# Kernel tuning notes

Hardware: AMD Instinct MI355X
Metric: run time of the kernel (lower is better)

The kernel has to match this reference:

```python
import jax, jax.numpy as jnp
import numpy as np

B, S, HIDDEN = 2, 2048, 1024
NUM_HEADS, HEAD_DIM = 16, 64
STRIDE = 128
NEG = -10000.0


def _strided_mask(seq_len):
    # Sparse Transformer strided pattern: causal, local window of STRIDE,
    # plus every STRIDE-th previous position.
    i = jnp.arange(seq_len)[:, None]
    j = jnp.arange(seq_len)[None, :]
    diff = i - j
    allowed = (diff >= 0) & ((diff < STRIDE) | (diff % STRIDE == 0))
    return jnp.where(allowed, 0.0, NEG).astype(jnp.float32)  # [S, S]


def setup_inputs() -> dict:
    key = jax.random.key(0)
    k0, k1, k2, k3, k4 = jax.random.split(key, 5)
    hidden_states = jax.random.normal(k0, (B, S, HIDDEN), dtype=jnp.float32)
    attention_mask = jnp.zeros((B, 1, 1, S), dtype=jnp.float32)
    W_q = jax.random.normal(k1, (HIDDEN, HIDDEN), dtype=jnp.float32) * 0.02
    b_q = jnp.zeros((HIDDEN,), dtype=jnp.float32)
    W_v = jax.random.normal(k2, (HIDDEN, HIDDEN), dtype=jnp.float32) * 0.02
    b_v = jnp.zeros((HIDDEN,), dtype=jnp.float32)
    return {"hidden_states": hidden_states, "attention_mask": attention_mask,
            "W_q": W_q, "b_q": b_q, "W_v": W_v, "b_v": b_v}


def _heads(x):
    b, s, _ = x.shape
    return x.reshape(b, s, NUM_HEADS, HEAD_DIM).transpose(0, 2, 1, 3)  # [B,H,S,d]


def reference(hidden_states, attention_mask, W_q, b_q, W_v, b_v):
    q = _heads(hidden_states @ W_q + b_q)  # [B,H,S,d]
    v = _heads(hidden_states @ W_v + b_v)  # [B,H,S,d]
    hash_mask = _strided_mask(q.shape[-2])  # [S,S], broadcast over B,H
    # NB: source computes matmul(query, query^T) -- Q used for both sides.
    scores = jnp.einsum('bhid,bhjd->bhij', q, q) + hash_mask
    scores = scores / jnp.sqrt(jnp.asarray(HEAD_DIM, scores.dtype))
    scores = scores + attention_mask
    probs = jax.nn.softmax(scores, axis=-1)  # dropout p=0 (eval)
    ctx = jnp.einsum('bhij,bhjd->bhid', probs, v)  # [B,H,S,d]
    b = ctx.shape[0]
    return ctx.transpose(0, 2, 1, 3).reshape(b, -1, NUM_HEADS * HEAD_DIM)
```

## Files before the change

kernel.cpp:

```cpp
#include <hip/hip_runtime.h>

typedef __attribute__((ext_vector_type(8))) short short8;
typedef __attribute__((ext_vector_type(4))) float float4v;

__device__ inline float bf2f(ushort u) {
    unsigned v = ((unsigned)u) << 16;
    return __builtin_bit_cast(float, v);
}
__device__ inline ushort f2bf(float f) {
    unsigned u = __builtin_bit_cast(unsigned, f);
    u += 0x7FFFu + ((u >> 16) & 1u);
    return (ushort)(u >> 16);
}

__device__ inline void gload_lds16(const ushort* g, ushort* l) {
    __builtin_amdgcn_global_load_lds(
        (const __attribute__((address_space(1))) unsigned int*)g,
        (__attribute__((address_space(3))) unsigned int*)l,
        16, 0, 0);
}

__global__ __launch_bounds__(256) void prep(
    const float* __restrict__ hs, ushort* __restrict__ hsb,
    const float* __restrict__ Wq, const float* __restrict__ Wv,
    ushort* __restrict__ Wt) {
    __shared__ ushort tile[64][68];
    if (blockIdx.x < 1024) {
        const size_t base = ((size_t)blockIdx.x * 256 + threadIdx.x) * 16;
        union { ushort u[16]; uint4 v[2]; } o;
#pragma unroll
        for (int q = 0; q < 4; ++q) {
            float4v f = *(const float4v*)(hs + base + q * 4);
#pragma unroll
            for (int j = 0; j < 4; ++j) o.u[q * 4 + j] = f2bf(f[j]);
        }
        *(uint4*)(hsb + base)     = o.v[0];
        *(uint4*)(hsb + base + 8) = o.v[1];
        return;
    }
    const int idx = blockIdx.x - 1024;
    const int z = idx >> 8, yy = (idx >> 4) & 15, xx = idx & 15;
    const float* W = z ? Wv : Wq;
    ushort* Wto    = Wt + (z ? (size_t)1024 * 1024 : 0);
    const int k0 = yy * 64, n0 = xx * 64;
    const int tid = threadIdx.x;
    const int rr = tid >> 4;
    const int cc = (tid & 15) * 4;
    union U4 { ushort u[4]; uint2 v; };
#pragma unroll
    for (int i = 0; i < 4; ++i) {
        int row = rr + i * 16;
        float4v f = *(const float4v*)(W + (size_t)(k0 + row) * 1024 + n0 + cc);
        U4 x;
#pragma unroll
        for (int j = 0; j < 4; ++j) x.u[j] = f2bf(f[j]);
        *(uint2*)&tile[row][cc] = x.v;
    }
    __syncthreads();
#pragma unroll
    for (int i = 0; i < 4; ++i) {
        int row = rr + i * 16;
        U4 o;
#pragma unroll
        for (int j = 0; j < 4; ++j) o.u[j] = tile[cc + j][row];
        *(uint2*)(Wto + (size_t)(n0 + row) * 1024 + k0 + cc) = o.v;
    }
}

__global__ __launch_bounds__(512, 2) void qv_gemm(
    const ushort* __restrict__ hsb, const ushort* __restrict__ Wt,
    const float* __restrict__ bq, const float* __restrict__ bv,
    ushort* __restrict__ q_ws, ushort* __restrict__ v_ws) {
    __shared__ ushort smem[73728];
    const int wg = blockIdx.x;
    const int n0 = (wg & 7) * 256;
    const int m0 = (wg >> 3) * 128;
    const int tid  = threadIdx.x;
    const int wid  = tid >> 6, lane = tid & 63;
    const int quad = lane >> 4, l16 = lane & 15;
    const int wm = (wid >> 2) * 64;
    const int wn = (wid & 3) * 64;
    const int srow8 = tid >> 3;
    const int scb   = (tid & 7) * 16;

    auto stage = [&](int ktt, int bi, int r) {
        if (r < 2) {
            int row = r * 64 + srow8;
            int sb  = scb ^ ((row & 7) << 4);
            gload_lds16(hsb + (size_t)(m0 + row) * 1024 + ktt * 64 + (sb >> 1),
                        (ushort*)((char*)smem + bi * 49152 + r * 8192 + wid * 1024));
        } else {
            int row = (r - 2) * 64 + srow8;
            int sb  = scb ^ ((row & 7) << 4);
            gload_lds16(Wt + (size_t)(n0 + row) * 1024 + ktt * 64 + (sb >> 1),
                        (ushort*)((char*)smem + bi * 49152 + 16384 + (r - 2) * 8192 + wid * 1024));
        }
    };

    float4v acc[4][4] = {};

#pragma unroll
    for (int r = 0; r < 6; ++r) stage(0, 0, r);
#pragma unroll
    for (int r = 0; r < 6; ++r) stage(1, 1, r);

    int bi = 0;
    for (int ktt = 0; ktt < 16; ++ktt) {
        const char* Ab = (const char*)smem + bi * 49152;
        const char* Bb = Ab + 16384;

        if (ktt < 15) asm volatile("s_waitcnt vmcnt(6)" ::: "memory");
        else          asm volatile("s_waitcnt vmcnt(0)" ::: "memory");
        __builtin_amdgcn_s_barrier();
        __builtin_amdgcn_sched_barrier(0);

        short8 af[4][2], bfr[4][2];
#pragma unroll
        for (int mt = 0; mt < 4; ++mt) {
            int ar = wm + mt * 16 + l16;
            int sw = (ar & 7) << 4;
            af[mt][0] = *(const short8*)(Ab + ar * 128 + ((quad * 16) ^ sw));
        }
#pragma unroll
        for (int nt = 0; nt < 4; ++nt) {
            int br = wn + nt * 16 + l16;
            int sw = (br & 7) << 4;
            bfr[nt][0] = *(const short8*)(Bb + br * 128 + ((quad * 16) ^ sw));
        }
        __builtin_amdgcn_sched_barrier(0);
        const int kn = ktt + 2;
        const int b2 = (bi + 2 >= 3) ? bi - 1 : bi + 2;
        if (kn < 16) {
            stage(kn, b2, 0); stage(kn, b2, 1); stage(kn, b2, 2);
            stage(kn, b2, 3); stage(kn, b2, 4); stage(kn, b2, 5);
        }
#pragma unroll
        for (int mt = 0; mt < 4; ++mt) {
            int ar = wm + mt * 16 + l16;
            int sw = (ar & 7) << 4;
            af[mt][1] = *(const short8*)(Ab + ar * 128 + (((4 + quad) * 16) ^ sw));
        }
#pragma unroll
        for (int nt = 0; nt < 4; ++nt) {
            int br = wn + nt * 16 + l16;
            int sw = (br & 7) << 4;
            bfr[nt][1] = *(const short8*)(Bb + br * 128 + (((4 + quad) * 16) ^ sw));
        }
        __builtin_amdgcn_sched_barrier(0);
        asm volatile("s_waitcnt lgkmcnt(8)" ::: "memory");
        __builtin_amdgcn_sched_barrier(0);
        __builtin_amdgcn_s_setprio(1);
#pragma unroll
        for (int mt = 0; mt < 4; ++mt)
#pragma unroll
            for (int nt = 0; nt < 4; ++nt)
                acc[mt][nt] = __builtin_amdgcn_mfma_f32_16x16x32_bf16(
                    af[mt][0], bfr[nt][0], acc[mt][nt], 0, 0, 0);
        __builtin_amdgcn_s_setprio(0);
        asm volatile("s_waitcnt lgkmcnt(0)" ::: "memory");
        __builtin_amdgcn_sched_barrier(0);
        __builtin_amdgcn_s_setprio(1);
#pragma unroll
        for (int mt = 0; mt < 4; ++mt)
#pragma unroll
            for (int nt = 0; nt < 4; ++nt)
                acc[mt][nt] = __builtin_amdgcn_mfma_f32_16x16x32_bf16(
                    af[mt][1], bfr[nt][1], acc[mt][nt], 0, 0, 0);
        __builtin_amdgcn_s_setprio(0);

        bi = (bi + 1 >= 3) ? 0 : bi + 1;
    }

#pragma unroll
    for (int mt = 0; mt < 4; ++mt) {
#pragma unroll
        for (int nt = 0; nt < 4; ++nt) {
            int coln = n0 + wn + nt * 16 + l16;
            bool isq = coln < 1024;
            int c2 = isq ? coln : coln - 1024;
            float bsv = isq ? bq[c2] : bv[c2];
            ushort* outp = isq ? q_ws : v_ws;
            int hh = c2 >> 6, dd = c2 & 63;
#pragma unroll
            for (int reg = 0; reg < 4; ++reg) {
                int r = m0 + wm + mt * 16 + quad * 4 + reg;
                int bb = r >> 11, s = r & 2047;
                outp[(((size_t)bb * 16 + hh) * 2048 + s) * 64 + dd] =
                    f2bf(acc[mt][nt][reg] + bsv);
            }
        }
    }
}

#define SISSUE(As, Bs, Ms, idx) { const ushort* kr_ = q_ws + srbase + ((size_t)(idx) << 13); \
    As = *(const uint4*)kr_; Bs = *(const uint4*)(kr_ + 8); Ms = amask[amrow + ((idx) << 7)]; }
#define SCONS(As, Bs, Ms, kk) { union { uint4 v; ushort u[8]; } t0_, t1_; t0_.v = As; t1_.v = Bs; \
    float p_ = 0.f; \
    _Pragma("unroll") for (int jj = 0; jj < 8; ++jj) p_ += qv[jj] * bf2f(t0_.u[jj]); \
    _Pragma("unroll") for (int jj = 0; jj < 8; ++jj) p_ += qv[8 + jj] * bf2f(t1_.u[jj]); \
    p_ += __shfl_xor(p_, 1); p_ += __shfl_xor(p_, 2); \
    if ((tid & 3) == 0) Sstr[sr][kk] = p_ * 0.125f + Ms; }
#define VISSUE(As, Bs, idx) { const ushort* vr_ = v_ws + srbase + ((size_t)(idx) << 13); \
    As = *(const uint4*)vr_; Bs = *(const uint4*)(vr_ + 8); }
#define VCONS(As, Bs, kk) { float p_ = Sstr[sr][kk]; union { uint4 v; ushort u[8]; } t0_, t1_; \
    t0_.v = As; t1_.v = Bs; \
    _Pragma("unroll") for (int jj = 0; jj < 8; ++jj) acc16[jj] += p_ * bf2f(t0_.u[jj]); \
    _Pragma("unroll") for (int jj = 0; jj < 8; ++jj) acc16[8 + jj] += p_ * bf2f(t1_.u[jj]); }

__global__ __launch_bounds__(512, 4) void attn(
    const ushort* __restrict__ q_ws, const ushort* __restrict__ v_ws,
    const float* __restrict__ amask, float* __restrict__ out) {
    const int wg = blockIdx.x;
    const int half = wg >> 8, r5 = wg & 255;
    const int t_raw = r5 & 15;
    const int t = half ? (15 - t_raw) : t_raw;
    const int h = r5 >> 4;
    const int b = half;

    __shared__ ushort KwPl[16384];
    __shared__ ushort VtS[16384];
    __shared__ float  Sstr[128][17];
    __shared__ float  amw[256];

    const int tid = threadIdx.x;
    const int wid = tid >> 6, lane = tid & 63;
    const int quad = lane >> 4, l16 = lane & 15;
    const int r0 = wid * 16;
    const size_t qbase = ((size_t)b * 16 + h) * 2048 * 64;
    const int base_row = (t - 1) * 128;
    const int nk = (t >= 2) ? (t - 1) : 0;

    const int sr = tid >> 2;
    const int dq = (tid & 3) * 16;
    const size_t srbase = qbase + (size_t)sr * 64 + dq;
    const size_t amrow  = (size_t)b * 2048 + sr;

#pragma unroll
    for (int i = 0; i < 4; ++i) {
        int u = tid + i * 512;
        int row = u >> 3, c = u & 7;
        int jg = base_row + row; if (jg < 0) jg = 0;
        int sc = c ^ (row & 7);
        gload_lds16(q_ws + qbase + (size_t)jg * 64 + sc * 8, &KwPl[u * 8]);
    }
    __builtin_amdgcn_sched_barrier(0);

    {
        const int vj = tid & 255, dh0 = (tid >> 8) * 32;
        int vjg = base_row + vj; if (vjg < 0) vjg = 0;
        const ushort* vsrc = v_ws + qbase + (size_t)vjg * 64 + dh0;
        int cj = vj >> 3, j7 = vj & 7;
#pragma unroll
        for (int d0 = 0; d0 < 32; d0 += 8) {
            union { uint4 v; ushort u[8]; } tmp;
            tmp.v = *(const uint4*)(vsrc + d0);
#pragma unroll
            for (int jj = 0; jj < 8; ++jj) {
                int dd = dh0 + d0 + jj;
                VtS[dd * 256 + ((cj ^ (dd & 7)) * 8) + j7] = tmp.u[jj];
            }
        }
        int amj = base_row + (tid & 255); if (amj < 0) amj = 0;
        amw[tid & 255] = amask[(size_t)b * 2048 + amj];
    }

    uint4 kA0{}, kB0{}, kA1{}, kB1{}, kA2{}, kB2{};
    float am0 = 0.f, am1 = 0.f, am2 = 0.f;
    if (nk > 0) {
        SISSUE(kA0, kB0, am0, 0);
        SISSUE(kA1, kB1, am1, (1 < nk ? 1 : 0));
        SISSUE(kA2, kB2, am2, (2 < nk ? 2 : 0));
    }

    asm volatile("s_waitcnt vmcnt(0) lgkmcnt(0)" ::: "memory");
    __builtin_amdgcn_s_barrier();
    __builtin_amdgcn_sched_barrier(0);

    if (nk > 0) {
        float qv[16];
#pragma unroll
        for (int cc = 0; cc < 2; ++cc) {
            int c = (dq >> 3) + cc;
            union { uint4 v; ushort u[8]; } tm;
            tm.v = *(const uint4*)&KwPl[(128 + sr) * 64 + ((c ^ (sr & 7)) * 8)];
#pragma unroll
            for (int jj = 0; jj < 8; ++jj) qv[cc * 8 + jj] = bf2f(tm.u[jj]);
        }
        for (int k = 0; k < nk; k += 3) {
            SCONS(kA0, kB0, am0, k);
            if (k + 3 < nk) SISSUE(kA0, kB0, am0, k + 3);
            if (k + 1 < nk) {
                SCONS(kA1, kB1, am1, k + 1);
                if (k + 4 < nk) SISSUE(kA1, kB1, am1, k + 4);
            }
            if (k + 2 < nk) {
                SCONS(kA2, kB2, am2, k + 2);
                if (k + 5 < nk) SISSUE(kA2, kB2, am2, k + 5);
            }
        }
    }

    float4v sacc[16] = {};
    __builtin_amdgcn_s_setprio(1);
#pragma unroll
    for (int ks = 0; ks < 2; ++ks) {
        int c = ks * 4 + quad;
        int sw = (c ^ (l16 & 7)) * 8;
        short8 af = *(const short8*)&KwPl[(128 + r0 + l16) * 64 + sw];
#pragma unroll
        for (int nt = 0; nt < 16; ++nt) {
            short8 bfr = *(const short8*)&KwPl[(nt * 16 + l16) * 64 + sw];
            sacc[nt] = __builtin_amdgcn_mfma_f32_16x16x32_bf16(af, bfr, sacc[nt], 0, 0, 0);
        }
    }
    __builtin_amdgcn_s_setprio(0);
    __syncthreads();

    unsigned pb[4][4];
#pragma unroll
    for (int reg = 0; reg < 4; ++reg) {
        int rr = r0 + quad * 4 + reg;
        float sstr_v = (l16 < nk) ? Sstr[rr][l16] : -INFINITY;
        float m = sstr_v;
#pragma unroll
        for (int nt = 0; nt < 16; ++nt) {
            int c = nt * 16 + l16;
            bool allowed = (c >= rr) && (c <= rr + 128) && (t > 0 || c >= 128);
            float x = allowed ? sacc[nt][reg] * 0.125f + amw[c] : -INFINITY;
            sacc[nt][reg] = x;
            m = fmaxf(m, x);
        }
#pragma unroll
        for (int off = 1; off < 16; off <<= 1) m = fmaxf(m, __shfl_xor(m, off));

        float es = (l16 < nk) ? __expf(sstr_v - m) : 0.f;
        float sum = es;
#pragma unroll
        for (int nt = 0; nt < 16; ++nt) {
            float x = sacc[nt][reg];
            float e = (x == -INFINITY) ? 0.f : __expf(x - m);
            sacc[nt][reg] = e; sum += e;
        }
#pragma unroll
        for (int off = 1; off < 16; off <<= 1) sum += __shfl_xor(sum, off);
        float rden = 1.f / sum;
#pragma unroll
        for (int nt = 0; nt < 8; ++nt) {
            int c = nt * 2 + (l16 >> 3);
            KwPl[rr * 128 + ((c ^ (rr & 15)) * 8) + (l16 & 7)] = f2bf(sacc[nt][reg] * rden);
        }
#pragma unroll
        for (int i2 = 0; i2 < 4; ++i2) {
            unsigned lo = f2bf(sacc[8 + 2 * i2][reg] * rden);
            unsigned hi = f2bf(sacc[9 + 2 * i2][reg] * rden);
            pb[reg][i2] = lo | (hi << 16);
        }
        if (l16 < nk) Sstr[rr][l16] = es * rden;
    }
    __syncthreads();

    uint4 vA0{}, vB0{}, vA1{}, vB1{}, vA2{}, vB2{};
    if (nk > 0) {
        VISSUE(vA0, vB0, 0);
        VISSUE(vA1, vB1, (1 < nk ? 1 : 0));
        VISSUE(vA2, vB2, (2 < nk ? 2 : 0));
    }

    float4v cacc[4] = {};
    __builtin_amdgcn_s_setprio(1);
#pragma unroll
    for (int ks = 0; ks < 4; ++ks) {
        int cp = ks * 4 + quad;
        short8 af = *(const short8*)&KwPl[(r0 + l16) * 128 + ((cp ^ l16) * 8)];
#pragma unroll
        for (int nt = 0; nt < 4; ++nt) {
            int sw = (cp ^ (l16 & 7)) * 8;
            short8 bfr = *(const short8*)&VtS[(nt * 16 + l16) * 256 + sw];
            cacc[nt] = __builtin_amdgcn_mfma_f32_16x16x32_bf16(af, bfr, cacc[nt], 0, 0, 0);
        }
    }
    __builtin_amdgcn_s_setprio(0);
    __syncthreads();

#pragma unroll
    for (int reg = 0; reg < 4; ++reg) {
        int rr = r0 + quad * 4 + reg;
#pragma unroll
        for (int i2 = 0; i2 < 4; ++i2) {
            int nt0 = 8 + 2 * i2;
#pragma unroll
            for (int e2 = 0; e2 < 2; ++e2) {
                int nt = nt0 + e2;
                int c = (nt - 8) * 2 + (l16 >> 3);
                ushort val = (ushort)((pb[reg][i2] >> (16 * e2)) & 0xFFFF);
                KwPl[rr * 128 + ((c ^ (rr & 15)) * 8) + (l16 & 7)] = val;
            }
        }
    }
    __syncthreads();

    __builtin_amdgcn_s_setprio(1);
#pragma unroll
    for (int ks = 0; ks < 4; ++ks) {
        int cp = ks * 4 + quad;
        short8 af = *(const short8*)&KwPl[(r0 + l16) * 128 + ((cp ^ l16) * 8)];
#pragma unroll
        for (int nt = 0; nt < 4; ++nt) {
            int cv = 16 + cp;
            int sw = (cv ^ (l16 & 7)) * 8;
            short8 bfr = *(const short8*)&VtS[(nt * 16 + l16) * 256 + sw];
            cacc[nt] = __builtin_amdgcn_mfma_f32_16x16x32_bf16(af, bfr, cacc[nt], 0, 0, 0);
        }
    }
    __builtin_amdgcn_s_setprio(0);

    float acc16[16] = {};
    if (nk > 0) {
        for (int k = 0; k < nk; k += 3) {
            VCONS(vA0, vB0, k);
            if (k + 3 < nk) VISSUE(vA0, vB0, k + 3);
            if (k + 1 < nk) {
                VCONS(vA1, vB1, k + 1);
                if (k + 4 < nk) VISSUE(vA1, vB1, k + 4);
            }
            if (k + 2 < nk) {
                VCONS(vA2, vB2, k + 2);
                if (k + 5 < nk) VISSUE(vA2, vB2, k + 5);
            }
        }
    }
    __syncthreads();

    float* ctxp = (float*)&VtS[0];
#pragma unroll
    for (int d4 = 0; d4 < 4; ++d4) {
        int c = (dq >> 2) + d4;
        *(float4v*)&ctxp[sr * 64 + ((c ^ (sr & 15)) * 4)] =
            *(const float4v*)&acc16[d4 * 4];
    }
    __syncthreads();

    const size_t obase = ((size_t)b * 2048 + (size_t)t * 128) * 1024 + (size_t)h * 64;
#pragma unroll
    for (int nt = 0; nt < 4; ++nt)
#pragma unroll
        for (int reg = 0; reg < 4; ++reg) {
            int rr = r0 + quad * 4 + reg;
            int d = nt * 16 + l16;
            float cstr = ctxp[rr * 64 + (((d >> 2) ^ (rr & 15)) * 4) + (d & 3)];
            out[obase + (size_t)rr * 1024 + d] = cacc[nt][reg] + cstr;
        }
}

extern "C" void kernel_launch(void* const* d_in, const int* in_sizes, int n_in,
                              void* d_out, int out_size, void* d_ws, size_t ws_size,
                              hipStream_t stream) {
    int ihs = -1, iam = -1, iw1 = -1, iw2 = -1, ib1 = -1, ib2 = -1;
    for (int i = 0; i < n_in; ++i) {
        int s = in_sizes[i];
        if      (s == 4194304) { if (ihs < 0) ihs = i; }
        else if (s == 4096)    { if (iam < 0) iam = i; }
        else if (s == 1048576) { if (iw1 < 0) iw1 = i; else if (iw2 < 0) iw2 = i; }
        else if (s == 1024)    { if (ib1 < 0) ib1 = i; else if (ib2 < 0) ib2 = i; }
    }
    if (ihs < 0) ihs = 0; if (iam < 0) iam = 1;
    if (iw1 < 0) iw1 = 2; if (ib1 < 0) ib1 = 3;
    if (iw2 < 0) iw2 = 4; if (ib2 < 0) ib2 = 5;

    const float* hs    = (const float*)d_in[ihs];
    const float* amask = (const float*)d_in[iam];
    const float* Wq    = (const float*)d_in[iw1];
    const float* bq    = (const float*)d_in[ib1];
    const float* Wv    = (const float*)d_in[iw2];
    const float* bv    = (const float*)d_in[ib2];
    float* out = (float*)d_out;

    char* ws = (char*)d_ws;
    ushort* Wt   = (ushort*)(ws);
    ushort* hsb  = (ushort*)(ws + (1u << 22));
    ushort* q_ws = (ushort*)(ws + (1u << 22) + (1u << 23));
    ushort* v_ws = (ushort*)(ws + (1u << 22) + (2u << 23));

    prep<<<1536, 256, 0, stream>>>(hs, hsb, Wq, Wv, Wt);
    qv_gemm<<<256, 512, 0, stream>>>(hsb, Wt, bq, bv, q_ws, v_ws);
    attn<<<512, 512, 0, stream>>>(q_ws, v_ws, amask, out);
}
```

Baseline: 132.6 us.

## Split QV projection GEMM k-step into interleaved quadrant phases with staggered prefetch

Restructures the inner k-loop of the fused Q/V projection GEMM into four quadrant phases. Each phase loads a subset of A/B fragments from LDS, issues a third of the global-to-LDS prefetch for tile k+2, and runs its MFMAs behind block barriers, in a ping-pong style schedule. The aim is to spread LDS reads and global loads across the MFMA work so they overlap more evenly and stall less. In exchange it adds three extra s_barriers and full lgkmcnt(0) waits per iteration, which could serialize the waves.

```diff
diff --git a/kernel.cpp b/kernel.cpp
--- a/kernel.cpp
+++ b/kernel.cpp
@@ -108,6 +108,9 @@
     for (int ktt = 0; ktt < 16; ++ktt) {
         const char* Ab = (const char*)smem + bi * 49152;
         const char* Bb = Ab + 16384;
+        const int kn = ktt + 2;
+        const int b2 = (bi + 2 >= 3) ? bi - 1 : bi + 2;
+        const bool pf = (kn < 16);
 
         if (ktt < 15) asm volatile("s_waitcnt vmcnt(6)" ::: "memory");
         else          asm volatile("s_waitcnt vmcnt(0)" ::: "memory");
@@ -115,57 +118,94 @@
         __builtin_amdgcn_sched_barrier(0);
 
         short8 af[4][2], bfr[4][2];
-#pragma unroll
-        for (int mt = 0; mt < 4; ++mt) {
+
+#pragma unroll
+        for (int mt = 0; mt < 2; ++mt) {
             int ar = wm + mt * 16 + l16;
             int sw = (ar & 7) << 4;
             af[mt][0] = *(const short8*)(Ab + ar * 128 + ((quad * 16) ^ sw));
-        }
-#pragma unroll
-        for (int nt = 0; nt < 4; ++nt) {
+            af[mt][1] = *(const short8*)(Ab + ar * 128 + (((4 + quad) * 16) ^ sw));
+        }
+#pragma unroll
+        for (int nt = 0; nt < 2; ++nt) {
             int br = wn + nt * 16 + l16;
             int sw = (br & 7) << 4;
             bfr[nt][0] = *(const short8*)(Bb + br * 128 + ((quad * 16) ^ sw));
-        }
-        __builtin_amdgcn_sched_barrier(0);
-        const int kn = ktt + 2;
-        const int b2 = (bi + 2 >= 3) ? bi - 1 : bi + 2;
-        if (kn < 16) {
-            stage(kn, b2, 0); stage(kn, b2, 1); stage(kn, b2, 2);
-            stage(kn, b2, 3); stage(kn, b2, 4); stage(kn, b2, 5);
-        }
-#pragma unroll
-        for (int mt = 0; mt < 4; ++mt) {
+            bfr[nt][1] = *(const short8*)(Bb + br * 128 + (((4 + quad) * 16) ^ sw));
+        }
+        if (pf) { stage(kn, b2, 0); stage(kn, b2, 1); }
+        __builtin_amdgcn_sched_barrier(0);
+        __builtin_amdgcn_s_barrier();
+        asm volatile("s_waitcnt lgkmcnt(0)" ::: "memory");
+        __builtin_amdgcn_sched_barrier(0);
+        __builtin_amdgcn_s_setprio(1);
+#pragma unroll
+        for (int ks = 0; ks < 2; ++ks)
+#pragma unroll
+            for (int mt = 0; mt < 2; ++mt)
+#pragma unroll
+                for (int nt = 0; nt < 2; ++nt)
+                    acc[mt][nt] = __builtin_amdgcn_mfma_f32_16x16x32_bf16(
+                        af[mt][ks], bfr[nt][ks], acc[mt][nt], 0, 0, 0);
+        __builtin_amdgcn_s_setprio(0);
+        __builtin_amdgcn_sched_barrier(0);
+        __builtin_amdgcn_s_barrier();
+
+#pragma unroll
+        for (int nt = 2; nt < 4; ++nt) {
+            int br = wn + nt * 16 + l16;
+            int sw = (br & 7) << 4;
+            bfr[nt][0] = *(const short8*)(Bb + br * 128 + ((quad * 16) ^ sw));
+            bfr[nt][1] = *(const short8*)(Bb + br * 128 + (((4 + quad) * 16) ^ sw));
+        }
+        if (pf) { stage(kn, b2, 2); stage(kn, b2, 3); }
+        __builtin_amdgcn_sched_barrier(0);
+        __builtin_amdgcn_s_barrier();
+        asm volatile("s_waitcnt lgkmcnt(0)" ::: "memory");
+        __builtin_amdgcn_sched_barrier(0);
+        __builtin_amdgcn_s_setprio(1);
+#pragma unroll
+        for (int ks = 0; ks < 2; ++ks)
+#pragma unroll
+            for (int mt = 0; mt < 2; ++mt)
+#pragma unroll
+                for (int nt = 2; nt < 4; ++nt)
+                    acc[mt][nt] = __builtin_amdgcn_mfma_f32_16x16x32_bf16(
+                        af[mt][ks], bfr[nt][ks], acc[mt][nt], 0, 0, 0);
+        __builtin_amdgcn_s_setprio(0);
+        __builtin_amdgcn_sched_barrier(0);
+        __builtin_amdgcn_s_barrier();
+
+#pragma unroll
+        for (int mt = 2; mt < 4; ++mt) {
             int ar = wm + mt * 16 + l16;
             int sw = (ar & 7) << 4;
+            af[mt][0] = *(const short8*)(Ab + ar * 128 + ((quad * 16) ^ sw));
             af[mt][1] = *(const short8*)(Ab + ar * 128 + (((4 + quad) * 16) ^ sw));
         }
-#pragma unroll
-        for (int nt = 0; nt < 4; ++nt) {
-            int br = wn + nt * 16 + l16;
-            int sw = (br & 7) << 4;
-            bfr[nt][1] = *(const short8*)(Bb + br * 128 + (((4 + quad) * 16) ^ sw));
-        }
-        __builtin_amdgcn_sched_barrier(0);
-        asm volatile("s_waitcnt lgkmcnt(8)" ::: "memory");
+        if (pf) { stage(kn, b2, 4); stage(kn, b2, 5); }
+        __builtin_amdgcn_sched_barrier(0);
+        __builtin_amdgcn_s_barrier();
+        asm volatile("s_waitcnt lgkmcnt(0)" ::: "memory");
         __builtin_amdgcn_sched_barrier(0);
         __builtin_amdgcn_s_setprio(1);
 #pragma unroll
-        for (int mt = 0; mt < 4; ++mt)
-#pragma unroll
-            for (int nt = 0; nt < 4; ++nt)
-                acc[mt][nt] = __builtin_amdgcn_mfma_f32_16x16x32_bf16(
-                    af[mt][0], bfr[nt][0], acc[mt][nt], 0, 0, 0);
-        __builtin_amdgcn_s_setprio(0);
-        asm volatile("s_waitcnt lgkmcnt(0)" ::: "memory");
-        __builtin_amdgcn_sched_barrier(0);
-        __builtin_amdgcn_s_setprio(1);
-#pragma unroll
-        for (int mt = 0; mt < 4; ++mt)
-#pragma unroll
-            for (int nt = 0; nt < 4; ++nt)
-                acc[mt][nt] = __builtin_amdgcn_mfma_f32_16x16x32_bf16(
-                    af[mt][1], bfr[nt][1], acc[mt][nt], 0, 0, 0);
+        for (int ks = 0; ks < 2; ++ks)
+#pragma unroll
+            for (int mt = 2; mt < 4; ++mt)
+#pragma unroll
+                for (int nt = 0; nt < 2; ++nt)
+                    acc[mt][nt] = __builtin_amdgcn_mfma_f32_16x16x32_bf16(
+                        af[mt][ks], bfr[nt][ks], acc[mt][nt], 0, 0, 0);
+
+#pragma unroll
+        for (int ks = 0; ks < 2; ++ks)
+#pragma unroll
+            for (int mt = 2; mt < 4; ++mt)
+#pragma unroll
+                for (int nt = 2; nt < 4; ++nt)
+                    acc[mt][nt] = __builtin_amdgcn_mfma_f32_16x16x32_bf16(
+                        af[mt][ks], bfr[nt][ks], acc[mt][nt], 0, 0, 0);
         __builtin_amdgcn_s_setprio(0);
 
         bi = (bi + 1 >= 3) ? 0 : bi + 1;
```

After: 138.1 us. 4.1% more time.
